# Kernel optimization log

Hardware: AMD Instinct MI355X
Metric: run time of the kernel (lower is better)

## Reference

```python
import jax, jax.numpy as jnp
import numpy as np

B, DIN, H_DEC, LAT, NE, E = 16384, 8192, 256, 4, 4, 8
TAU = 1.0
LN_EPS = 1e-5


def _mish(x):
    return x * jnp.tanh(jax.nn.softplus(x))


def _ln(x):
    # LayerNorm over last dim, no affine params (elementwise_affine=False)
    m = jnp.mean(x, axis=-1, keepdims=True)
    v = jnp.mean(jnp.square(x - m), axis=-1, keepdims=True)
    return (x - m) * jax.lax.rsqrt(v + LN_EPS)


def _moe(x, gw, gb, w1, b1, w2, b2, w3, b3, w4, b4):
    # Batched version of the 8-expert Python loop: all experts in one grouped einsum.
    gate = jax.nn.softmax(x @ gw + gb, axis=-1)                 # [B, E]
    h = _ln(_mish(jnp.einsum('bd,edh->beh', x, w1) + b1))       # [B, E, H]
    h = _ln(_mish(jnp.einsum('beh,ehk->bek', h, w2) + b2))
    h = _mish(jnp.einsum('beh,ehk->bek', h, w3) + b3)
    out = jnp.einsum('beh,eho->beo', h, w4) + b4                # [B, E, O]
    return jnp.einsum('be,beo->bo', gate, out)                  # gate-weighted sum


def setup_inputs() -> dict:
    key = jax.random.key(0)
    ks = jax.random.split(key, 16)
    s = lambda k, shape: jax.random.normal(k, shape, jnp.float32) * 0.02
    return {
        'x': jax.random.normal(ks[0], (B, DIN), jnp.float32),
        'gumbel_u': jax.random.uniform(ks[1], (B, NE), jnp.float32),
        'codebook': jax.random.uniform(ks[2], (NE, LAT), jnp.float32, -1.0 / NE, 1.0 / NE),
        'enc_gate_w': s(ks[3], (DIN, E)), 'enc_gate_b': jnp.zeros((E,), jnp.float32),
        'enc_w1': s(ks[4], (E, DIN, LAT)), 'enc_b1': jnp.zeros((E, LAT), jnp.float32),
        'enc_w2': s(ks[5], (E, LAT, LAT)), 'enc_b2': jnp.zeros((E, LAT), jnp.float32),
        'enc_w3': s(ks[6], (E, LAT, LAT)), 'enc_b3': jnp.zeros((E, LAT), jnp.float32),
        'enc_w4': s(ks[7], (E, LAT, LAT)), 'enc_b4': jnp.zeros((E, LAT), jnp.float32),
        'dec_gate_w': s(ks[8], (NE, E)), 'dec_gate_b': jnp.zeros((E,), jnp.float32),
        'dec_w1': s(ks[9], (E, NE, H_DEC)), 'dec_b1': jnp.zeros((E, H_DEC), jnp.float32),
        'dec_w2': s(ks[10], (E, H_DEC, H_DEC)), 'dec_b2': jnp.zeros((E, H_DEC), jnp.float32),
        'dec_w3': s(ks[11], (E, H_DEC, H_DEC)), 'dec_b3': jnp.zeros((E, H_DEC), jnp.float32),
        'dec_w4': s(ks[12], (E, H_DEC, 8)), 'dec_b4': jnp.zeros((E, 8), jnp.float32),
    }


def reference(x, gumbel_u, codebook,
              enc_gate_w, enc_gate_b, enc_w1, enc_b1, enc_w2, enc_b2,
              enc_w3, enc_b3, enc_w4, enc_b4,
              dec_gate_w, dec_gate_b, dec_w1, dec_b1, dec_w2, dec_b2,
              dec_w3, dec_b3, dec_w4, dec_b4):
    # result=None inference path (eval mode -> dropout is identity)
    estimate = _moe(x, enc_gate_w, enc_gate_b, enc_w1, enc_b1, enc_w2, enc_b2,
                    enc_w3, enc_b3, enc_w4, enc_b4)               # [B, LAT]
    logits = estimate @ codebook.T                                # [B, NE]
    g = -jnp.log(-jnp.log(jnp.clip(gumbel_u, 1e-10, 1.0 - 1e-7)))
    y_soft = jax.nn.softmax((logits + g) / TAU, axis=-1)
    y_hard = jax.nn.one_hot(jnp.argmax(y_soft, axis=-1), NE, dtype=y_soft.dtype)
    one_hot = y_hard - jax.lax.stop_gradient(y_soft) + y_soft     # straight-through
    x_recon = _moe(one_hot, dec_gate_w, dec_gate_b, dec_w1, dec_b1, dec_w2, dec_b2,
                   dec_w3, dec_b3, dec_w4, dec_b4)                # [B, 8]
    return x_recon
```

## Files before the change

### kernel.cpp

```cpp
#include <hip/hip_runtime.h>
#include <hip/hip_bf16.h>
#include <cstdint>

#define B_ROWS 16384
#define DIN    8192
#define NE_    4
#define NEXP   8
#define HDEC   256
#define NCOL   40
#define CHUNK  256
#define NCHUNK (DIN / CHUNK)
#define RPB    8
#define CPW    5

typedef float f32x4 __attribute__((ext_vector_type(4)));

__device__ __forceinline__ float mishf(float x) {
    float sp = (x > 20.f) ? x : log1pf(expf(x));
    return x * tanhf(sp);
}
__device__ __forceinline__ double mishd(double x) {
    double sp = (x > 30.0) ? x : log1p(exp(x));
    return x * tanh(sp);
}
__device__ __forceinline__ void ln4d(const double* a, double* o) {
    double m  = (a[0] + a[1] + a[2] + a[3]) * 0.25;
    double d0 = a[0] - m, d1 = a[1] - m, d2 = a[2] - m, d3 = a[3] - m;
    double v  = (d0*d0 + d1*d1 + d2*d2 + d3*d3) * 0.25;
    double r  = 1.0 / sqrt(v + 1e-5);
    o[0] = d0*r; o[1] = d1*r; o[2] = d2*r; o[3] = d3*r;
}

__global__ __launch_bounds__(256) void sentinel_k(float* __restrict__ out, int n, float v) {
    int i = blockIdx.x * 256 + threadIdx.x;
    if (i < n) out[i] = v;
}

__global__ __launch_bounds__(256) void prep_w40t(const float* __restrict__ gw,
                                                 const float* __restrict__ w1,
                                                 float* __restrict__ w40t) {
    int idx = blockIdx.x * 256 + threadIdx.x;
    int j = idx >> 13, k = idx & (DIN - 1);
    float v;
    if (j < 8) {
        v = gw[k * 8 + j];
    } else {
        int e = (j - 8) >> 2, h = (j - 8) & 3;
        v = w1[((size_t)e * DIN + k) * 4 + h];
    }
    w40t[idx] = v;
}

__device__ __forceinline__ float blk_sum256(float v, volatile float* red) {
    #pragma unroll
    for (int off = 32; off > 0; off >>= 1) v += __shfl_down(v, off, 64);
    int lane = threadIdx.x & 63, w = threadIdx.x >> 6;
    if (lane == 0) red[w] = v;
    __syncthreads();
    float s = red[0] + red[1] + red[2] + red[3];
    __syncthreads();
    return s;
}

__global__ __launch_bounds__(256) void dec_expert(
    const float* __restrict__ w1, const float* __restrict__ b1,
    const float* __restrict__ w2, const float* __restrict__ b2,
    const float* __restrict__ w3, const float* __restrict__ b3,
    const float* __restrict__ w4, const float* __restrict__ b4,
    float* __restrict__ outE) {
    __shared__ float h[HDEC];
    __shared__ float red[4];
    int c = blockIdx.x >> 3, e = blockIdx.x & 7, t = threadIdx.x;

    float a   = mishf(w1[((size_t)e * NE_ + c) * HDEC + t] + b1[e * HDEC + t]);
    float m   = blk_sum256(a, red) * (1.f / HDEC);
    float d   = a - m;
    float var = blk_sum256(d * d, red) * (1.f / HDEC);
    h[t] = d * rsqrtf(var + 1e-5f);
    __syncthreads();

    float s = b2[e * HDEC + t];
    #pragma unroll 16
    for (int i = 0; i < HDEC; ++i) s += h[i] * w2[((size_t)e * HDEC + i) * HDEC + t];
    __syncthreads();
    a   = mishf(s);
    m   = blk_sum256(a, red) * (1.f / HDEC);
    d   = a - m;
    var = blk_sum256(d * d, red) * (1.f / HDEC);
    h[t] = d * rsqrtf(var + 1e-5f);
    __syncthreads();

    s = b3[e * HDEC + t];
    #pragma unroll 16
    for (int i = 0; i < HDEC; ++i) s += h[i] * w3[((size_t)e * HDEC + i) * HDEC + t];
    __syncthreads();
    float h3 = mishf(s);

    for (int j = 0; j < 8; ++j) {
        float oj = blk_sum256(h3 * w4[((size_t)e * HDEC + t) * 8 + j], red);
        if (t == 0) outE[((size_t)c * 8 + e) * 8 + j] = oj + b4[e * 8 + j];
    }
}

__global__ __launch_bounds__(512) void gemm_main(
    const float* __restrict__ x, const float* __restrict__ w40t,
    double* __restrict__ y)
{
    __shared__ float xbuf[2][RPB][CHUNK];

    const int t    = threadIdx.x;
    const int lane = t & 63;
    const int cg   = t >> 6;
    const int rowBase = blockIdx.x * RPB;
    const int j0   = cg * CPW;

    typedef const char __attribute__((address_space(1)))* gp_t;
    typedef char __attribute__((address_space(3)))* lp_t;

    const float* __restrict__ xsrc = x + (size_t)(rowBase + cg) * DIN + (lane << 2);
    const float* __restrict__ wr   = w40t + (size_t)j0 * DIN + (lane << 2);

    float acc[RPB][CPW];
    #pragma unroll
    for (int r = 0; r < RPB; ++r)
        #pragma unroll
        for (int jj = 0; jj < CPW; ++jj) acc[r][jj] = 0.f;

    __builtin_amdgcn_global_load_lds(
        (gp_t)(const void*)xsrc,
        (lp_t)(void*)(&xbuf[0][cg][lane << 2]), 16, 0, 0);
    __syncthreads();

    for (int c = 0; c < NCHUNK; ++c) {
        const int cur = c & 1;

        f32x4 wv0 = *(const f32x4*)(wr + (size_t)c * CHUNK);
        f32x4 wv1 = *(const f32x4*)(wr + (size_t)DIN     + (size_t)c * CHUNK);
        f32x4 wv2 = *(const f32x4*)(wr + 2 * (size_t)DIN + (size_t)c * CHUNK);
        f32x4 wv3 = *(const f32x4*)(wr + 3 * (size_t)DIN + (size_t)c * CHUNK);
        f32x4 wv4 = *(const f32x4*)(wr + 4 * (size_t)DIN + (size_t)c * CHUNK);
        __builtin_amdgcn_sched_barrier(0);

        if (c + 1 < NCHUNK)
            __builtin_amdgcn_global_load_lds(
                (gp_t)(const void*)(xsrc + (size_t)(c + 1) * CHUNK),
                (lp_t)(void*)(&xbuf[cur ^ 1][cg][lane << 2]), 16, 0, 0);
        __builtin_amdgcn_sched_barrier(0);

        #pragma unroll
        for (int r = 0; r < RPB; ++r) {
            f32x4 xv = *(const f32x4*)(&xbuf[cur][r][lane << 2]);
            float a0 = acc[r][0];
            a0 = fmaf(xv.x, wv0.x, a0); a0 = fmaf(xv.y, wv0.y, a0);
            a0 = fmaf(xv.z, wv0.z, a0); a0 = fmaf(xv.w, wv0.w, a0);
            acc[r][0] = a0;
            float a1 = acc[r][1];
            a1 = fmaf(xv.x, wv1.x, a1); a1 = fmaf(xv.y, wv1.y, a1);
            a1 = fmaf(xv.z, wv1.z, a1); a1 = fmaf(xv.w, wv1.w, a1);
            acc[r][1] = a1;
            float a2 = acc[r][2];
            a2 = fmaf(xv.x, wv2.x, a2); a2 = fmaf(xv.y, wv2.y, a2);
            a2 = fmaf(xv.z, wv2.z, a2); a2 = fmaf(xv.w, wv2.w, a2);
            acc[r][2] = a2;
            float a3 = acc[r][3];
            a3 = fmaf(xv.x, wv3.x, a3); a3 = fmaf(xv.y, wv3.y, a3);
            a3 = fmaf(xv.z, wv3.z, a3); a3 = fmaf(xv.w, wv3.w, a3);
            acc[r][3] = a3;
            float a4 = acc[r][4];
            a4 = fmaf(xv.x, wv4.x, a4); a4 = fmaf(xv.y, wv4.y, a4);
            a4 = fmaf(xv.z, wv4.z, a4); a4 = fmaf(xv.w, wv4.w, a4);
            acc[r][4] = a4;
        }

        __syncthreads();
    }

    #pragma unroll
    for (int r = 0; r < RPB; ++r) {
        #pragma unroll
        for (int jj = 0; jj < CPW; ++jj) {
            double v = (double)acc[r][jj];
            #pragma unroll
            for (int off = 32; off > 0; off >>= 1) v += __shfl_xor(v, off, 64);
            if (lane == 0) y[(size_t)(rowBase + r) * NCOL + (j0 + jj)] = v;
        }
    }
}

__global__ __launch_bounds__(256) void tail_k(
    const double* __restrict__ yg, const float* __restrict__ outE,
    const float* __restrict__ gu,  const float* __restrict__ cb,
    const float* __restrict__ egb, const float* __restrict__ eb1,
    const float* __restrict__ ew2, const float* __restrict__ eb2,
    const float* __restrict__ ew3, const float* __restrict__ eb3,
    const float* __restrict__ ew4, const float* __restrict__ eb4,
    const float* __restrict__ dgw, const float* __restrict__ dgb,
    float* __restrict__ out)
{
    const int row = blockIdx.x * 256 + threadIdx.x;
    const double* __restrict__ y = yg + (size_t)row * NCOL;

    double gv[8], mx = -1e300, gs = 0.0;
    #pragma unroll
    for (int e = 0; e < 8; ++e) { gv[e] = y[e] + (double)egb[e]; mx = fmax(mx, gv[e]); }
    #pragma unroll
    for (int e = 0; e < 8; ++e) { gv[e] = exp(gv[e] - mx); gs += gv[e]; }
    double inv = 1.0 / gs;

    double est[4] = {0, 0, 0, 0};
    #pragma unroll
    for (int e = 0; e < 8; ++e) {
        double a[4], l1[4], p2[4], l2[4], h3[4];
        #pragma unroll
        for (int hh = 0; hh < 4; ++hh)
            a[hh] = mishd(y[8 + e * 4 + hh] + (double)eb1[e * 4 + hh]);
        ln4d(a, l1);
        #pragma unroll
        for (int hh = 0; hh < 4; ++hh) {
            double s = (double)eb2[e * 4 + hh];
            #pragma unroll
            for (int i = 0; i < 4; ++i) s += l1[i] * (double)ew2[(e * 4 + i) * 4 + hh];
            p2[hh] = mishd(s);
        }
        ln4d(p2, l2);
        #pragma unroll
        for (int hh = 0; hh < 4; ++hh) {
            double s = (double)eb3[e * 4 + hh];
            #pragma unroll
            for (int i = 0; i < 4; ++i) s += l2[i] * (double)ew3[(e * 4 + i) * 4 + hh];
            h3[hh] = mishd(s);
        }
        double g = gv[e] * inv;
        #pragma unroll
        for (int hh = 0; hh < 4; ++hh) {
            double s = (double)eb4[e * 4 + hh];
            #pragma unroll
            for (int i = 0; i < 4; ++i) s += h3[i] * (double)ew4[(e * 4 + i) * 4 + hh];
            est[hh] += g * s;
        }
    }

    const double ulo = (double)1e-10f, uhi = (double)(1.0f - 1e-7f);
    double best = -1e300; int kb = 0;
    #pragma unroll
    for (int n = 0; n < 4; ++n) {
        double lg = 0.0;
        #pragma unroll
        for (int l = 0; l < 4; ++l) lg += est[l] * (double)cb[n * 4 + l];
        double u = (double)gu[(size_t)row * 4 + n];
        u = fmin(fmax(u, ulo), uhi);
        double z = lg - log(-log(u));
        if (z > best) { best = z; kb = n; }
    }

    double g2[8], mx2 = -1e300, gs2 = 0.0;
    #pragma unroll
    for (int e = 0; e < 8; ++e) {
        g2[e] = (double)dgw[kb * 8 + e] + (double)dgb[e];
        mx2 = fmax(mx2, g2[e]);
    }
    #pragma unroll
    for (int e = 0; e < 8; ++e) { g2[e] = exp(g2[e] - mx2); gs2 += g2[e]; }
    double inv2 = 1.0 / gs2;

    float o[8];
    #pragma unroll
    for (int j = 0; j < 8; ++j) {
        double s = 0.0;
        #pragma unroll
        for (int e = 0; e < 8; ++e)
            s += g2[e] * (double)outE[((size_t)kb * 8 + e) * 8 + j];
        o[j] = (float)(s * inv2);
    }
    float* op = out + (size_t)row * 8;
    *reinterpret_cast<float4*>(op)     = make_float4(o[0], o[1], o[2], o[3]);
    *reinterpret_cast<float4*>(op + 4) = make_float4(o[4], o[5], o[6], o[7]);
}

extern "C" void kernel_launch(void* const* d_in, const int* in_sizes, int n_in,
                              void* d_out, int out_size, void* d_ws, size_t ws_size,
                              hipStream_t stream) {
    float* out = (float*)d_out;

    static const int expect[23] = {
        B_ROWS * DIN, B_ROWS * NE_, NE_ * 4,
        DIN * NEXP, NEXP,
        NEXP * DIN * 4, NEXP * 4,
        NEXP * 16, NEXP * 4,
        NEXP * 16, NEXP * 4,
        NEXP * 16, NEXP * 4,
        NE_ * NEXP, NEXP,
        NEXP * NE_ * HDEC, NEXP * HDEC,
        NEXP * HDEC * HDEC, NEXP * HDEC,
        NEXP * HDEC * HDEC, NEXP * HDEC,
        NEXP * HDEC * 8, NEXP * 8
    };
    const size_t need = (size_t)(NCOL * DIN + 512) * sizeof(float)
                      + (size_t)B_ROWS * NCOL * sizeof(double);
    bool ok = (n_in == 23) && (out_size == B_ROWS * 8) && (ws_size >= need);
    if (ok) {
        for (int i = 0; i < 23; ++i) ok = ok && (in_sizes[i] == expect[i]);
    }
    if (!ok) {
        sentinel_k<<<(out_size + 255) / 256, 256, 0, stream>>>(out, out_size, 1.0e6f);
        return;
    }

    const float* x   = (const float*)d_in[0];
    const float* gu  = (const float*)d_in[1];
    const float* cb  = (const float*)d_in[2];
    const float* egw = (const float*)d_in[3];
    const float* egb = (const float*)d_in[4];
    const float* ew1 = (const float*)d_in[5];
    const float* eb1 = (const float*)d_in[6];
    const float* ew2 = (const float*)d_in[7];
    const float* eb2 = (const float*)d_in[8];
    const float* ew3 = (const float*)d_in[9];
    const float* eb3 = (const float*)d_in[10];
    const float* ew4 = (const float*)d_in[11];
    const float* eb4 = (const float*)d_in[12];
    const float* dgw = (const float*)d_in[13];
    const float* dgb = (const float*)d_in[14];
    const float* dw1 = (const float*)d_in[15];
    const float* db1 = (const float*)d_in[16];
    const float* dw2 = (const float*)d_in[17];
    const float* db2 = (const float*)d_in[18];
    const float* dw3 = (const float*)d_in[19];
    const float* db3 = (const float*)d_in[20];
    const float* dw4 = (const float*)d_in[21];
    const float* db4 = (const float*)d_in[22];

    float*  w40t = (float*)d_ws;
    float*  outE = w40t + (size_t)NCOL * DIN;
    double* yws  = (double*)(w40t + (size_t)NCOL * DIN + 512);

    prep_w40t <<<(NCOL * DIN) / 256, 256, 0, stream>>>(egw, ew1, w40t);
    dec_expert<<<NE_ * NEXP, 256, 0, stream>>>(dw1, db1, dw2, db2, dw3, db3,
                                               dw4, db4, outE);
    gemm_main <<<B_ROWS / RPB, 512, 0, stream>>>(x, w40t, yws);
    tail_k    <<<B_ROWS / 256, 256, 0, stream>>>(yws, outE, gu, cb, egb, eb1,
                                                 ew2, eb2, ew3, eb3, ew4, eb4,
                                                 dgw, dgb, out);
}
```

Measured before the change: 414.4 us.

## Split GEMM blocks across column halves and fuse prep kernels into one launch

The main GEMM now uses 256-thread blocks, twice as many as before, with each block computing 20 of the 40 output columns for 8 rows. Each wave now stages two x rows into LDS instead of one. The aim is more, smaller blocks for better occupancy and latency hiding, at the cost of each x row being fetched by two blocks, which relies on L2 to absorb the duplicate reads. Separately, the weight-transpose prep and the decoder-expert precompute are merged into one kernel launch to cut launch overhead.

```diff
diff --git a/kernel.cpp b/kernel.cpp
--- a/kernel.cpp
+++ b/kernel.cpp
@@ -12,6 +12,7 @@
 #define NCHUNK (DIN / CHUNK)
 #define RPB    8
 #define CPW    5
+#define PREP_BLOCKS ((NCOL * DIN) / 256)
 
 typedef float f32x4 __attribute__((ext_vector_type(4)));
 
@@ -36,21 +37,6 @@
     if (i < n) out[i] = v;
 }
 
-__global__ __launch_bounds__(256) void prep_w40t(const float* __restrict__ gw,
-                                                 const float* __restrict__ w1,
-                                                 float* __restrict__ w40t) {
-    int idx = blockIdx.x * 256 + threadIdx.x;
-    int j = idx >> 13, k = idx & (DIN - 1);
-    float v;
-    if (j < 8) {
-        v = gw[k * 8 + j];
-    } else {
-        int e = (j - 8) >> 2, h = (j - 8) & 3;
-        v = w1[((size_t)e * DIN + k) * 4 + h];
-    }
-    w40t[idx] = v;
-}
-
 __device__ __forceinline__ float blk_sum256(float v, volatile float* red) {
     #pragma unroll
     for (int off = 32; off > 0; off >>= 1) v += __shfl_down(v, off, 64);
@@ -62,15 +48,34 @@
     return s;
 }
 
-__global__ __launch_bounds__(256) void dec_expert(
-    const float* __restrict__ w1, const float* __restrict__ b1,
-    const float* __restrict__ w2, const float* __restrict__ b2,
-    const float* __restrict__ w3, const float* __restrict__ b3,
-    const float* __restrict__ w4, const float* __restrict__ b4,
-    float* __restrict__ outE) {
+__global__ __launch_bounds__(256) void prep_all(
+    const float* __restrict__ gw,  const float* __restrict__ ew1,
+    float* __restrict__ w40t,
+    const float* __restrict__ w1,  const float* __restrict__ b1,
+    const float* __restrict__ w2,  const float* __restrict__ b2,
+    const float* __restrict__ w3,  const float* __restrict__ b3,
+    const float* __restrict__ w4,  const float* __restrict__ b4,
+    float* __restrict__ outE)
+{
     __shared__ float h[HDEC];
     __shared__ float red[4];
-    int c = blockIdx.x >> 3, e = blockIdx.x & 7, t = threadIdx.x;
+
+    if (blockIdx.x < PREP_BLOCKS) {
+        int idx = blockIdx.x * 256 + threadIdx.x;
+        int j = idx >> 13, k = idx & (DIN - 1);
+        float v;
+        if (j < 8) {
+            v = gw[k * 8 + j];
+        } else {
+            int e = (j - 8) >> 2, hh = (j - 8) & 3;
+            v = ew1[((size_t)e * DIN + k) * 4 + hh];
+        }
+        w40t[idx] = v;
+        return;
+    }
+
+    int bid = blockIdx.x - PREP_BLOCKS;
+    int c = bid >> 3, e = bid & 7, t = threadIdx.x;
 
     float a   = mishf(w1[((size_t)e * NE_ + c) * HDEC + t] + b1[e * HDEC + t]);
     float m   = blk_sum256(a, red) * (1.f / HDEC);
@@ -102,7 +107,7 @@
     }
 }
 
-__global__ __launch_bounds__(512) void gemm_main(
+__global__ __launch_bounds__(256) void gemm_main(
     const float* __restrict__ x, const float* __restrict__ w40t,
     double* __restrict__ y)
 {
@@ -110,15 +115,17 @@
 
     const int t    = threadIdx.x;
     const int lane = t & 63;
-    const int cg   = t >> 6;
-    const int rowBase = blockIdx.x * RPB;
-    const int j0   = cg * CPW;
+    const int wv   = t >> 6;
+    const int bid  = blockIdx.x;
+    const int rowBase  = (bid >> 1) * RPB;
+    const int j0   = (bid & 1) * 20 + wv * CPW;
 
     typedef const char __attribute__((address_space(1)))* gp_t;
     typedef char __attribute__((address_space(3)))* lp_t;
 
-    const float* __restrict__ xsrc = x + (size_t)(rowBase + cg) * DIN + (lane << 2);
-    const float* __restrict__ wr   = w40t + (size_t)j0 * DIN + (lane << 2);
+    const float* __restrict__ xsrcA = x + (size_t)(rowBase + wv)     * DIN + (lane << 2);
+    const float* __restrict__ xsrcB = x + (size_t)(rowBase + wv + 4) * DIN + (lane << 2);
+    const float* __restrict__ wr    = w40t + (size_t)j0 * DIN + (lane << 2);
 
     float acc[RPB][CPW];
     #pragma unroll
@@ -127,8 +134,11 @@
         for (int jj = 0; jj < CPW; ++jj) acc[r][jj] = 0.f;
 
     __builtin_amdgcn_global_load_lds(
-        (gp_t)(const void*)xsrc,
-        (lp_t)(void*)(&xbuf[0][cg][lane << 2]), 16, 0, 0);
+        (gp_t)(const void*)xsrcA,
+        (lp_t)(void*)(&xbuf[0][wv][lane << 2]), 16, 0, 0);
+    __builtin_amdgcn_global_load_lds(
+        (gp_t)(const void*)xsrcB,
+        (lp_t)(void*)(&xbuf[0][wv + 4][lane << 2]), 16, 0, 0);
     __syncthreads();
 
     for (int c = 0; c < NCHUNK; ++c) {
@@ -141,10 +151,14 @@
         f32x4 wv4 = *(const f32x4*)(wr + 4 * (size_t)DIN + (size_t)c * CHUNK);
         __builtin_amdgcn_sched_barrier(0);
 
-        if (c + 1 < NCHUNK)
+        if (c + 1 < NCHUNK) {
             __builtin_amdgcn_global_load_lds(
-                (gp_t)(const void*)(xsrc + (size_t)(c + 1) * CHUNK),
-                (lp_t)(void*)(&xbuf[cur ^ 1][cg][lane << 2]), 16, 0, 0);
+                (gp_t)(const void*)(xsrcA + (size_t)(c + 1) * CHUNK),
+                (lp_t)(void*)(&xbuf[cur ^ 1][wv][lane << 2]), 16, 0, 0);
+            __builtin_amdgcn_global_load_lds(
+                (gp_t)(const void*)(xsrcB + (size_t)(c + 1) * CHUNK),
+                (lp_t)(void*)(&xbuf[cur ^ 1][wv + 4][lane << 2]), 16, 0, 0);
+        }
         __builtin_amdgcn_sched_barrier(0);
 
         #pragma unroll
@@ -334,11 +348,10 @@
     float*  outE = w40t + (size_t)NCOL * DIN;
     double* yws  = (double*)(w40t + (size_t)NCOL * DIN + 512);
 
-    prep_w40t <<<(NCOL * DIN) / 256, 256, 0, stream>>>(egw, ew1, w40t);
-    dec_expert<<<NE_ * NEXP, 256, 0, stream>>>(dw1, db1, dw2, db2, dw3, db3,
-                                               dw4, db4, outE);
-    gemm_main <<<B_ROWS / RPB, 512, 0, stream>>>(x, w40t, yws);
-    tail_k    <<<B_ROWS / 256, 256, 0, stream>>>(yws, outE, gu, cb, egb, eb1,
-                                                 ew2, eb2, ew3, eb3, ew4, eb4,
-                                                 dgw, dgb, out);
-}
+    prep_all <<<PREP_BLOCKS + NE_ * NEXP, 256, 0, stream>>>(
+        egw, ew1, w40t, dw1, db1, dw2, db2, dw3, db3, dw4, db4, outE);
+    gemm_main<<<(B_ROWS / RPB) * 2, 256, 0, stream>>>(x, w40t, yws);
+    tail_k   <<<B_ROWS / 256, 256, 0, stream>>>(yws, outE, gu, cb, egb, eb1,
+                                                ew2, eb2, ew3, eb3, ew4, eb4,
+                                                dgw, dgb, out);
+}
```

Result: faster. 394.0 us (-4.9%).
